# Optimization experiments

Hardware: AMD Instinct MI355X
Metric: run time of the kernel (lower is better)

Reference implementation:

```python
import jax, jax.numpy as jnp
import numpy as np

N_NODES = 20000
N_EDGES = 320000
DIMS = [256, 256, 128, 64]  # input_dim, hidden_dims...
EPS = 1e-5


def gcn_conv(x, w, b, src, dst, n):
    # PyG GCNConv: linear first, then symmetric-normalized aggregation with self-loops
    x = x @ w  # [N, out]
    loops = jnp.arange(n, dtype=src.dtype)
    src2 = jnp.concatenate([src, loops])
    dst2 = jnp.concatenate([dst, loops])
    deg = jax.ops.segment_sum(jnp.ones_like(dst2, dtype=x.dtype), dst2, num_segments=n)
    dinv = jnp.where(deg > 0, deg ** -0.5, 0.0)
    norm = dinv[src2] * dinv[dst2]  # [E+N]
    msg = x[src2] * norm[:, None]   # gathered, scaled messages
    out = jax.ops.segment_sum(msg, dst2, num_segments=n)
    return out + b


def graph_norm(x, w, b, a):
    # PyG GraphNorm over a single graph: per-feature mean/var across nodes
    mean = jnp.mean(x, axis=0)
    centered = x - a * mean
    var = jnp.mean(centered * centered, axis=0)
    return w * centered * jax.lax.rsqrt(var + EPS) + b


def layer_norm(x, w, b):
    mean = jnp.mean(x, axis=-1, keepdims=True)
    var = jnp.mean((x - mean) ** 2, axis=-1, keepdims=True)
    return (x - mean) * jax.lax.rsqrt(var + EPS) * w + b


def setup_inputs() -> dict:
    key = jax.random.key(0)
    ks = jax.random.split(key, 32)
    inp = {}
    inp["x"] = jax.random.normal(ks[0], (N_NODES, DIMS[0]), dtype=jnp.float32)
    inp["edge_index"] = jax.random.randint(ks[1], (2, N_EDGES), 0, N_NODES, dtype=jnp.int32)
    ki = 2
    for i in range(3):
        fin, fout = DIMS[i], DIMS[i + 1]
        s = 1.0 / np.sqrt(fin)
        inp[f"w{i}"] = jax.random.uniform(ks[ki], (fin, fout), jnp.float32, -s, s); ki += 1
        inp[f"b{i}"] = jnp.zeros((fout,), jnp.float32)
        inp[f"gn{i}_w"] = jnp.ones((fout,), jnp.float32)
        inp[f"gn{i}_b"] = jnp.zeros((fout,), jnp.float32)
        inp[f"gn{i}_a"] = jnp.ones((fout,), jnp.float32)
    h = DIMS[-1]
    s = 1.0 / np.sqrt(3 * h)
    inp["wc1"] = jax.random.uniform(ks[ki], (3 * h, h), jnp.float32, -s, s); ki += 1
    inp["bc1"] = jnp.zeros((h,), jnp.float32)
    inp["ln_w"] = jnp.ones((h,), jnp.float32)
    inp["ln_b"] = jnp.zeros((h,), jnp.float32)
    s = 1.0 / np.sqrt(h)
    inp["wc2"] = jax.random.uniform(ks[ki], (h, 2), jnp.float32, -s, s); ki += 1
    inp["bc2"] = jnp.zeros((2,), jnp.float32)
    return inp


def reference(x, edge_index,
              w0, b0, gn0_w, gn0_b, gn0_a,
              w1, b1, gn1_w, gn1_b, gn1_a,
              w2, b2, gn2_w, gn2_b, gn2_a,
              wc1, bc1, ln_w, ln_b, wc2, bc2):
    src, dst = edge_index[0], edge_index[1]
    n = x.shape[0]
    params = [(w0, b0, gn0_w, gn0_b, gn0_a),
              (w1, b1, gn1_w, gn1_b, gn1_a),
              (w2, b2, gn2_w, gn2_b, gn2_a)]
    for (w, b, gw, gb, ga) in params:
        x_res = x
        x = gcn_conv(x, w, b, src, dst, n)
        x = graph_norm(x, gw, gb, ga)
        x = jax.nn.gelu(x, approximate=False)
        # dropout = identity (eval); residual only when shapes match (layer 0)
        if x.shape == x_res.shape:
            x = x + x_res
    # multi-pool over the single graph (batch vector of zeros): mean | max | sum
    pooled = jnp.concatenate([jnp.mean(x, axis=0), jnp.max(x, axis=0), jnp.sum(x, axis=0)])[None, :]  # [1, 3h]
    h = pooled @ wc1 + bc1
    h = layer_norm(h, ln_w, ln_b)
    h = jax.nn.gelu(h, approximate=False)
    return h @ wc2 + bc2  # [1, num_classes]
```

## Files before the change

### kernel.cpp

```cpp
#include <hip/hip_runtime.h>
#include <math.h>

#define EPSV 1e-5f
#define MAXB 2176
#define GBLK 2080

typedef __attribute__((ext_vector_type(8))) short short8;
typedef __attribute__((ext_vector_type(4))) float f32x4;

__device__ __forceinline__ float gelu_f(float x) {
    return 0.5f * x * (1.0f + erff(x * 0.70710678118654752440f));
}

__device__ __forceinline__ float4 f4add(float4 a, float4 b) {
    return make_float4(a.x + b.x, a.y + b.y, a.z + b.z, a.w + b.w);
}

__device__ __forceinline__ ushort f2bf(float v) {
    union { float f; unsigned u; } a; a.f = v;
    unsigned r = a.u + 0x7FFFu + ((a.u >> 16) & 1u);
    return (ushort)(r >> 16);
}
__device__ __forceinline__ float bf2f(ushort h) {
    union { unsigned u; float f; } a; a.u = ((unsigned)h) << 16;
    return a.f;
}
__device__ __forceinline__ float4 bf4f(ushort4 v) {
    return make_float4(bf2f(v.x), bf2f(v.y), bf2f(v.z), bf2f(v.w));
}
__device__ __forceinline__ void f8_to_bf(const float* f, short8& h, short8& l) {
    union { short8 v; ushort u[8]; } H, L;
#pragma unroll
    for (int j = 0; j < 8; ++j) {
        H.u[j] = f2bf(f[j]);
        L.u[j] = f2bf(f[j] - bf2f(H.u[j]));
    }
    h = H.v; l = L.v;
}

__global__ void deg_kernel(const int* __restrict__ ei, int* __restrict__ deg, int E) {
    int stride = gridDim.x * blockDim.x;
    for (int e = blockIdx.x * blockDim.x + threadIdx.x; e < E; e += stride)
        atomicAdd(&deg[ei[E + e]], 1);
}

__global__ __launch_bounds__(1024) void scan_kernel(const int* __restrict__ deg,
                                                    int* __restrict__ off,
                                                    float* __restrict__ dinv, int N) {
    __shared__ int sh[1024];
    int t = threadIdx.x;
    int chunk = (N + 1023) >> 10;
    int b = t * chunk;
    int e = b + chunk; if (e > N) e = N;
    int s = 0;
    for (int i = b; i < e; ++i) s += deg[i];
    sh[t] = s;
    __syncthreads();
    for (int d = 1; d < 1024; d <<= 1) {
        int v = (t >= d) ? sh[t - d] : 0;
        __syncthreads();
        sh[t] += v;
        __syncthreads();
    }
    int run = (t > 0) ? sh[t - 1] : 0;
    for (int i = b; i < e; ++i) {
        off[i] = run;
        run += deg[i];
        dinv[i] = rsqrtf((float)(deg[i] + 1));
    }
    if (t == 1023) off[N] = sh[1023];
}

__global__ void fill_kernel(const int* __restrict__ ei, const int* __restrict__ off,
                            int* __restrict__ fill, int* __restrict__ csr, int E) {
    int stride = gridDim.x * blockDim.x;
    for (int e = blockIdx.x * blockDim.x + threadIdx.x; e < E; e += stride) {
        int d = ei[E + e];
        int p = off[d] + atomicAdd(&fill[d], 1);
        csr[p] = ei[e];
    }
}

__global__ void packw_all_kernel(const float* __restrict__ w0, const float* __restrict__ w1,
                                 const float* __restrict__ w2,
                                 ushort* __restrict__ wthi, ushort* __restrict__ wtlo)
{
    int idx = blockIdx.x * 256 + threadIdx.x;
    const float* W; int K, F, base, local;
    if (idx < 65536)       { W = w0; K = 256; F = 256; base = 0;     local = idx; }
    else if (idx < 98304)  { W = w1; K = 256; F = 128; base = 65536; local = idx - 65536; }
    else if (idx < 106496) { W = w2; K = 128; F = 64;  base = 98304; local = idx - 98304; }
    else return;
    int k = local / F, f = local - k * F;
    float v = W[local];
    ushort h = f2bf(v);
    wthi[base + f * K + k] = h;
    wtlo[base + f * K + k] = f2bf(v - bf2f(h));
}

template<int K, int BN, int MODE>
__global__ __launch_bounds__(256) void gemm_mfma_kernel(
    const float* __restrict__ axf,
    const ushort* __restrict__ tsrc,
    const float* __restrict__ tm, const float* __restrict__ tis,
    const float* __restrict__ tgw, const float* __restrict__ tgb,
    const float* __restrict__ tga, const float* __restrict__ res,
    const ushort* __restrict__ wthi, const ushort* __restrict__ wtlo,
    const float* __restrict__ dinv, ushort* __restrict__ C,
    int M, int F)
{
    constexpr int BM = 128, BK = 64;
    constexpr int LDK = BK + 8;
    constexpr int CF  = BN / 32;
    constexpr int WCH = BN / 32;

    __shared__ ushort AsH[BM * LDK], AsL[BM * LDK];
    __shared__ ushort WsH[BN * LDK], WsL[BN * LDK];

    const int tid = threadIdx.x;
    const int l = tid & 63, w = tid >> 6;
    const int wr = w >> 1, wc = w & 1;
    const int m0   = blockIdx.y * BM;
    const int colB = blockIdx.x * BN;
    const int lr = l & 15, lkg = l >> 4;

    f32x4 acc[4][CF] = {};

    for (int kk = 0; kk < K; kk += BK) {
        short8 ra[4], rb[4], rwh[WCH], rwl[WCH];
#pragma unroll
        for (int i = 0; i < 4; ++i) {
            int q = tid + i * 256;
            int row = q >> 3, cc = q & 7;
            int rg = m0 + row; if (rg > M - 1) rg = M - 1;
            int kc = kk + cc * 8;
            float y[8];
            if constexpr (MODE == 0) {
                const float* xp = axf + (size_t)rg * K + kc;
                float4 v0 = *(const float4*)xp, v1 = *(const float4*)(xp + 4);
                y[0]=v0.x; y[1]=v0.y; y[2]=v0.z; y[3]=v0.w;
                y[4]=v1.x; y[5]=v1.y; y[6]=v1.z; y[7]=v1.w;
            } else {
                const ushort* tp = tsrc + (size_t)rg * K + kc;
                float4 v0 = bf4f(*(const ushort4*)tp);
                float4 v1 = bf4f(*(const ushort4*)(tp + 4));
                float4 m0v = *(const float4*)(tm + kc),  m1v = *(const float4*)(tm + kc + 4);
                float4 i0v = *(const float4*)(tis + kc), i1v = *(const float4*)(tis + kc + 4);
                float4 w0v = *(const float4*)(tgw + kc), w1v = *(const float4*)(tgw + kc + 4);
                float4 b0v = *(const float4*)(tgb + kc), b1v = *(const float4*)(tgb + kc + 4);
                float4 a0v = *(const float4*)(tga + kc), a1v = *(const float4*)(tga + kc + 4);
                y[0] = gelu_f(w0v.x * (v0.x - a0v.x * m0v.x) * i0v.x + b0v.x);
                y[1] = gelu_f(w0v.y * (v0.y - a0v.y * m0v.y) * i0v.y + b0v.y);
                y[2] = gelu_f(w0v.z * (v0.z - a0v.z * m0v.z) * i0v.z + b0v.z);
                y[3] = gelu_f(w0v.w * (v0.w - a0v.w * m0v.w) * i0v.w + b0v.w);
                y[4] = gelu_f(w1v.x * (v1.x - a1v.x * m1v.x) * i1v.x + b1v.x);
                y[5] = gelu_f(w1v.y * (v1.y - a1v.y * m1v.y) * i1v.y + b1v.y);
                y[6] = gelu_f(w1v.z * (v1.z - a1v.z * m1v.z) * i1v.z + b1v.z);
                y[7] = gelu_f(w1v.w * (v1.w - a1v.w * m1v.w) * i1v.w + b1v.w);
                if (res) {
                    const float* rp = res + (size_t)rg * K + kc;
                    float4 r0 = *(const float4*)rp, r1 = *(const float4*)(rp + 4);
                    y[0] += r0.x; y[1] += r0.y; y[2] += r0.z; y[3] += r0.w;
                    y[4] += r1.x; y[5] += r1.y; y[6] += r1.z; y[7] += r1.w;
                }
            }
            f8_to_bf(y, ra[i], rb[i]);
        }
#pragma unroll
        for (int i = 0; i < WCH; ++i) {
            int q = tid + i * 256;
            int row = q >> 3, cc = q & 7;
            rwh[i] = *(const short8*)(wthi + (size_t)(colB + row) * K + kk + cc * 8);
            rwl[i] = *(const short8*)(wtlo + (size_t)(colB + row) * K + kk + cc * 8);
        }
        __syncthreads();
#pragma unroll
        for (int i = 0; i < 4; ++i) {
            int q = tid + i * 256;
            int row = q >> 3, cc = q & 7;
            *(short8*)&AsH[row * LDK + cc * 8] = ra[i];
            *(short8*)&AsL[row * LDK + cc * 8] = rb[i];
        }
#pragma unroll
        for (int i = 0; i < WCH; ++i) {
            int q = tid + i * 256;
            int row = q >> 3, cc = q & 7;
            *(short8*)&WsH[row * LDK + cc * 8] = rwh[i];
            *(short8*)&WsL[row * LDK + cc * 8] = rwl[i];
        }
        __syncthreads();

#pragma unroll
        for (int ks = 0; ks < 2; ++ks) {
            const int kof = ks * 32 + lkg * 8;
            short8 afh[4], afl[4];
#pragma unroll
            for (int rf = 0; rf < 4; ++rf) {
                int row = wr * 64 + rf * 16 + lr;
                afh[rf] = *(const short8*)&AsH[row * LDK + kof];
                afl[rf] = *(const short8*)&AsL[row * LDK + kof];
            }
            short8 wfh[CF], wfl[CF];
#pragma unroll
            for (int cf = 0; cf < CF; ++cf) {
                int row = wc * (BN / 2) + cf * 16 + lr;
                wfh[cf] = *(const short8*)&WsH[row * LDK + kof];
                wfl[cf] = *(const short8*)&WsL[row * LDK + kof];
            }
#pragma unroll
            for (int rf = 0; rf < 4; ++rf) {
#pragma unroll
                for (int cf = 0; cf < CF; ++cf) {
                    acc[rf][cf] = __builtin_amdgcn_mfma_f32_16x16x32_bf16(afh[rf], wfh[cf], acc[rf][cf], 0, 0, 0);
                    acc[rf][cf] = __builtin_amdgcn_mfma_f32_16x16x32_bf16(afh[rf], wfl[cf], acc[rf][cf], 0, 0, 0);
                    acc[rf][cf] = __builtin_amdgcn_mfma_f32_16x16x32_bf16(afl[rf], wfh[cf], acc[rf][cf], 0, 0, 0);
                }
            }
        }
    }

#pragma unroll
    for (int rf = 0; rf < 4; ++rf) {
#pragma unroll
        for (int j = 0; j < 4; ++j) {
            int r = m0 + wr * 64 + rf * 16 + lkg * 4 + j;
            if (r < M) {
                float dv = dinv[r];
                ushort* Cp = C + (size_t)r * F + colB + wc * (BN / 2) + lr;
#pragma unroll
                for (int cf = 0; cf < CF; ++cf)
                    Cp[cf * 16] = f2bf(acc[rf][cf][j] * dv);
            }
        }
    }
}

template<int F>
__global__ __launch_bounds__(256) void gather_kernel(
    const ushort* __restrict__ hs, const int* __restrict__ off,
    const int* __restrict__ csr, const float* __restrict__ dinv,
    const float* __restrict__ bias, ushort* __restrict__ t,
    float* __restrict__ p1, float* __restrict__ p2, int N)
{
    constexpr int NG  = F / 64;
    constexpr int NPB = 16;
    const int lane = threadIdx.x & 15;
    const int slot = threadIdx.x >> 4;

    const int xs    = blockIdx.x & 7;
    const int g     = xs % NG;
    const int r     = xs / NG;
    const int chunk = blockIdx.x >> 3;
    const int repl  = 8 / NG;
    const int nPerG = (int)(gridDim.x >> 3) * repl;
    const int j     = chunk * repl + r;

    const int col4 = g * 16 + lane;
    const int c0 = col4 * 4;
    const float4 bv = ((const float4*)bias)[col4];

    float4 a1 = make_float4(0.f, 0.f, 0.f, 0.f);
    float4 a2 = make_float4(0.f, 0.f, 0.f, 0.f);

    for (int d = j * NPB + slot; d < N; d += nPerG * NPB) {
        float4 acc = bf4f(*(const ushort4*)(hs + (size_t)d * F + c0));
        const int e0 = off[d], e1 = off[d + 1];
        int e = e0;
        for (; e + 8 <= e1; e += 8) {
            int s0 = csr[e + 0], s1 = csr[e + 1], s2 = csr[e + 2], s3 = csr[e + 3];
            int s4 = csr[e + 4], s5 = csr[e + 5], s6 = csr[e + 6], s7 = csr[e + 7];
            ushort4 v0 = *(const ushort4*)(hs + (size_t)s0 * F + c0);
            ushort4 v1 = *(const ushort4*)(hs + (size_t)s1 * F + c0);
            ushort4 v2 = *(const ushort4*)(hs + (size_t)s2 * F + c0);
            ushort4 v3 = *(const ushort4*)(hs + (size_t)s3 * F + c0);
            ushort4 v4 = *(const ushort4*)(hs + (size_t)s4 * F + c0);
            ushort4 v5 = *(const ushort4*)(hs + (size_t)s5 * F + c0);
            ushort4 v6 = *(const ushort4*)(hs + (size_t)s6 * F + c0);
            ushort4 v7 = *(const ushort4*)(hs + (size_t)s7 * F + c0);
            float4 u0 = f4add(bf4f(v0), bf4f(v1));
            float4 u1 = f4add(bf4f(v2), bf4f(v3));
            float4 u2 = f4add(bf4f(v4), bf4f(v5));
            float4 u3 = f4add(bf4f(v6), bf4f(v7));
            acc = f4add(acc, f4add(f4add(u0, u1), f4add(u2, u3)));
        }
        for (; e + 2 <= e1; e += 2) {
            int s0 = csr[e + 0], s1 = csr[e + 1];
            ushort4 v0 = *(const ushort4*)(hs + (size_t)s0 * F + c0);
            ushort4 v1 = *(const ushort4*)(hs + (size_t)s1 * F + c0);
            acc = f4add(acc, f4add(bf4f(v0), bf4f(v1)));
        }
        if (e < e1) {
            acc = f4add(acc, bf4f(*(const ushort4*)(hs + (size_t)csr[e] * F + c0)));
        }

        float dv = dinv[d];
        float4 o;
        o.x = fmaf(dv, acc.x, bv.x);
        o.y = fmaf(dv, acc.y, bv.y);
        o.z = fmaf(dv, acc.z, bv.z);
        o.w = fmaf(dv, acc.w, bv.w);
        ushort4 ov;
        ov.x = f2bf(o.x); ov.y = f2bf(o.y); ov.z = f2bf(o.z); ov.w = f2bf(o.w);
        *(ushort4*)(t + (size_t)d * F + c0) = ov;
        a1.x += o.x; a1.y += o.y; a1.z += o.z; a1.w += o.w;
        a2.x += o.x * o.x; a2.y += o.y * o.y; a2.z += o.z * o.z; a2.w += o.w * o.w;
    }

    __shared__ float red[8][256];
    red[0][threadIdx.x] = a1.x; red[1][threadIdx.x] = a1.y;
    red[2][threadIdx.x] = a1.z; red[3][threadIdx.x] = a1.w;
    red[4][threadIdx.x] = a2.x; red[5][threadIdx.x] = a2.y;
    red[6][threadIdx.x] = a2.z; red[7][threadIdx.x] = a2.w;
    __syncthreads();
    if (slot == 0) {
        float sum[8];
#pragma unroll
        for (int k = 0; k < 8; ++k) {
            float s = red[k][lane];
            for (int jj = 1; jj < NPB; ++jj) s += red[k][jj * 16 + lane];
            sum[k] = s;
        }
        ((float4*)p1)[(long)col4 * MAXB + blockIdx.x] = make_float4(sum[0], sum[1], sum[2], sum[3]);
        ((float4*)p2)[(long)col4 * MAXB + blockIdx.x] = make_float4(sum[4], sum[5], sum[6], sum[7]);
    }
}

__global__ __launch_bounds__(256) void statreduce_kernel(
    const float* __restrict__ p1, const float* __restrict__ p2,
    const float* __restrict__ ga,
    float* __restrict__ meanv, float* __restrict__ istdv,
    int nb, int N, int NG)
{
    const int c4 = blockIdx.x;
    const int g = (c4 >> 4) % NG;
    const float4* p14 = (const float4*)p1 + (long)c4 * MAXB;
    const float4* p24 = (const float4*)p2 + (long)c4 * MAXB;
    float4 a1 = make_float4(0.f, 0.f, 0.f, 0.f);
    float4 a2 = make_float4(0.f, 0.f, 0.f, 0.f);
    for (int r = threadIdx.x; r < nb; r += 256) {
        if (((r & 7) % NG) != g) continue;
        float4 v1 = p14[r];
        float4 v2 = p24[r];
        a1.x += v1.x; a1.y += v1.y; a1.z += v1.z; a1.w += v1.w;
        a2.x += v2.x; a2.y += v2.y; a2.z += v2.z; a2.w += v2.w;
    }
#pragma unroll
    for (int offv = 32; offv > 0; offv >>= 1) {
        a1.x += __shfl_down(a1.x, offv); a1.y += __shfl_down(a1.y, offv);
        a1.z += __shfl_down(a1.z, offv); a1.w += __shfl_down(a1.w, offv);
        a2.x += __shfl_down(a2.x, offv); a2.y += __shfl_down(a2.y, offv);
        a2.z += __shfl_down(a2.z, offv); a2.w += __shfl_down(a2.w, offv);
    }
    __shared__ float4 sh1[4], sh2[4];
    const int wid = threadIdx.x >> 6;
    if ((threadIdx.x & 63) == 0) { sh1[wid] = a1; sh2[wid] = a2; }
    __syncthreads();
    if (threadIdx.x == 0) {
        float4 t1 = sh1[0], t2 = sh2[0];
        for (int jj = 1; jj < 4; ++jj) {
            float4 u1 = sh1[jj], u2 = sh2[jj];
            t1.x += u1.x; t1.y += u1.y; t1.z += u1.z; t1.w += u1.w;
            t2.x += u2.x; t2.y += u2.y; t2.z += u2.z; t2.w += u2.w;
        }
        float s1a[4] = { t1.x, t1.y, t1.z, t1.w };
        float s2a[4] = { t2.x, t2.y, t2.z, t2.w };
#pragma unroll
        for (int k = 0; k < 4; ++k) {
            int c = c4 * 4 + k;
            float m = s1a[k] / (float)N;
            float a = ga[c];
            float var = s2a[k] / (float)N - 2.f * a * m * m + a * a * m * m;
            meanv[c] = m;
            istdv[c] = rsqrtf(var + EPSV);
        }
    }
}

__device__ __forceinline__ void atomicMaxFloat(float* addr, float val) {
    unsigned* ua = (unsigned*)addr;
    unsigned old = *ua;
    while (true) {
        float of = __uint_as_float(old);
        if (of >= val) break;
        unsigned assumed = old;
        old = atomicCAS(ua, assumed, __float_as_uint(val));
        if (old == assumed) break;
    }
}

__global__ void initpool_kernel(float* __restrict__ psum, float* __restrict__ pmax) {
    int t = threadIdx.x;
    psum[t] = 0.f;
    pmax[t] = -INFINITY;
}

__global__ __launch_bounds__(256) void colpool_ng_kernel(
    const ushort* __restrict__ t, const float* __restrict__ meanv,
    const float* __restrict__ istdv, const float* __restrict__ gw,
    const float* __restrict__ gb, const float* __restrict__ ga,
    float* __restrict__ psum, float* __restrict__ pmax,
    int M, int rowsPerBlock)
{
    int c = threadIdx.x & 63;
    int rl = threadIdx.x >> 6;
    int r0 = blockIdx.x * rowsPerBlock;
    int rend = r0 + rowsPerBlock; if (rend > M) rend = M;
    const float mc = meanv[c], ic = istdv[c], wc_ = gw[c], bc_ = gb[c], ac = ga[c];
    float a1 = 0.f, am = -INFINITY;
    for (int r = r0 + rl; r < rend; r += 4) {
        float v = bf2f(t[(long)r * 64 + c]);
        float y = gelu_f(wc_ * (v - ac * mc) * ic + bc_);
        a1 += y; am = fmaxf(am, y);
    }
    __shared__ float sh1[256], shm[256];
    sh1[threadIdx.x] = a1; shm[threadIdx.x] = am;
    __syncthreads();
    if (threadIdx.x < 64) {
        for (int j = 1; j < 4; ++j) {
            a1 += sh1[c + j * 64];
            am = fmaxf(am, shm[c + j * 64]);
        }
        atomicAdd(&psum[c], a1);
        atomicMaxFloat(&pmax[c], am);
    }
}

__global__ void head_kernel(const float* __restrict__ psum, const float* __restrict__ pmax,
                            const float* __restrict__ wc1, const float* __restrict__ bc1,
                            const float* __restrict__ lnw, const float* __restrict__ lnb,
                            const float* __restrict__ wc2, const float* __restrict__ bc2,
                            float* __restrict__ out, int M)
{
    __shared__ float p[192];
    int t = threadIdx.x;
    float s = psum[t];
    p[t] = s / (float)M;
    p[64 + t] = pmax[t];
    p[128 + t] = s;
    __syncthreads();
    float h = bc1[t];
    for (int k = 0; k < 192; ++k) h = fmaf(p[k], wc1[k * 64 + t], h);
    float m = h;
    for (int off = 32; off > 0; off >>= 1) m += __shfl_xor(m, off);
    m *= (1.f / 64.f);
    float d = h - m;
    float v = d * d;
    for (int off = 32; off > 0; off >>= 1) v += __shfl_xor(v, off);
    v *= (1.f / 64.f);
    float y = d * rsqrtf(v + EPSV) * lnw[t] + lnb[t];
    y = gelu_f(y);
    float o0 = y * wc2[t * 2 + 0];
    float o1 = y * wc2[t * 2 + 1];
    for (int off = 32; off > 0; off >>= 1) {
        o0 += __shfl_xor(o0, off);
        o1 += __shfl_xor(o1, off);
    }
    if (t == 0) {
        out[0] = o0 + bc2[0];
        out[1] = o1 + bc2[1];
    }
}

extern "C" void kernel_launch(void* const* d_in, const int* in_sizes, int n_in,
                              void* d_out, int out_size, void* d_ws, size_t ws_size,
                              hipStream_t stream)
{
    const float* x    = (const float*)d_in[0];
    const int*   ei   = (const int*)d_in[1];
    const float* w0   = (const float*)d_in[2];
    const float* b0   = (const float*)d_in[3];
    const float* gn0w = (const float*)d_in[4];
    const float* gn0b = (const float*)d_in[5];
    const float* gn0a = (const float*)d_in[6];
    const float* w1   = (const float*)d_in[7];
    const float* b1   = (const float*)d_in[8];
    const float* gn1w = (const float*)d_in[9];
    const float* gn1b = (const float*)d_in[10];
    const float* gn1a = (const float*)d_in[11];
    const float* w2   = (const float*)d_in[12];
    const float* b2   = (const float*)d_in[13];
    const float* gn2w = (const float*)d_in[14];
    const float* gn2b = (const float*)d_in[15];
    const float* gn2a = (const float*)d_in[16];
    const float* wc1  = (const float*)d_in[17];
    const float* bc1  = (const float*)d_in[18];
    const float* lnw  = (const float*)d_in[19];
    const float* lnb  = (const float*)d_in[20];
    const float* wc2  = (const float*)d_in[21];
    const float* bc2  = (const float*)d_in[22];

    const int N = in_sizes[0] / 256;
    const int E = in_sizes[1] / 2;

    float* ws = (float*)d_ws;
    const size_t BIG = (size_t)N * 256;
    ushort* HS   = (ushort*)ws;
    ushort* T    = (ushort*)(ws + BIG);
    float* dinv  = ws + 2 * BIG;
    int*   deg   = (int*)(dinv + N);
    int*   fill  = deg + N;
    int*   off   = fill + N;
    int*   csr   = off + N + 1;
    float* p1    = (float*)(csr + E);
    float* p2    = p1 + (size_t)64 * MAXB * 4;
    float* meanv = p2 + (size_t)64 * MAXB * 4;
    float* istdv = meanv + 256;
    float* psum  = istdv + 256;
    float* pmax  = psum + 64;
    ushort* wthi = (ushort*)(pmax + 64);
    ushort* wtlo = wthi + 106496;
    const int woff[3] = { 0, 65536, 98304 };

    hipMemsetAsync(deg, 0, (size_t)2 * N * sizeof(int), stream);
    deg_kernel<<<1024, 256, 0, stream>>>(ei, deg, E);
    scan_kernel<<<1, 1024, 0, stream>>>(deg, off, dinv, N);
    fill_kernel<<<1024, 256, 0, stream>>>(ei, off, fill, csr, E);
    packw_all_kernel<<<416, 256, 0, stream>>>(w0, w1, w2, wthi, wtlo);

    struct Layer {
        const float *b, *gw, *gb, *ga;
        int K, F;
    } L[3] = {
        { b0, gn0w, gn0b, gn0a, 256, 256 },
        { b1, gn1w, gn1b, gn1a, 256, 128 },
        { b2, gn2w, gn2b, gn2a, 128,  64 },
    };

    const int rowTiles = (N + 127) / 128;

    gemm_mfma_kernel<256, 128, 0><<<dim3(2, rowTiles), 256, 0, stream>>>(
        x, nullptr, nullptr, nullptr, nullptr, nullptr, nullptr, nullptr,
        wthi + woff[0], wtlo + woff[0], dinv, HS, N, 256);
    gather_kernel<256><<<GBLK, 256, 0, stream>>>(HS, off, csr, dinv, L[0].b, T, p1, p2, N);
    statreduce_kernel<<<64, 256, 0, stream>>>(p1, p2, L[0].ga, meanv, istdv, GBLK, N, 4);

    gemm_mfma_kernel<256, 128, 1><<<dim3(1, rowTiles), 256, 0, stream>>>(
        nullptr, T, meanv, istdv, L[0].gw, L[0].gb, L[0].ga, x,
        wthi + woff[1], wtlo + woff[1], dinv, HS, N, 128);
    gather_kernel<128><<<GBLK, 256, 0, stream>>>(HS, off, csr, dinv, L[1].b, T, p1, p2, N);
    statreduce_kernel<<<32, 256, 0, stream>>>(p1, p2, L[1].ga, meanv, istdv, GBLK, N, 2);

    gemm_mfma_kernel<128, 64, 1><<<dim3(1, rowTiles), 256, 0, stream>>>(
        nullptr, T, meanv, istdv, L[1].gw, L[1].gb, L[1].ga, nullptr,
        wthi + woff[2], wtlo + woff[2], dinv, HS, N, 64);
    gather_kernel<64><<<GBLK, 256, 0, stream>>>(HS, off, csr, dinv, L[2].b, T, p1, p2, N);
    statreduce_kernel<<<16, 256, 0, stream>>>(p1, p2, L[2].ga, meanv, istdv, GBLK, N, 1);

    initpool_kernel<<<1, 64, 0, stream>>>(psum, pmax);
    colpool_ng_kernel<<<(N + 127) / 128, 256, 0, stream>>>(
        T, meanv, istdv, L[2].gw, L[2].gb, L[2].ga, psum, pmax, N, 128);
    head_kernel<<<1, 64, 0, stream>>>(psum, pmax, wc1, bc1, lnw, lnb, wc2, bc2,
                                      (float*)d_out, N);
}
```

Measured before the change: 275.0 us.

## Drop activation low-bf16 split in GEMM and merge small setup kernels

The GEMM no longer splits activations into high and low bf16 parts. It keeps only the high part, removing one of the three MFMA products per tile along with the AsL shared buffer and its stores. Separately, the CSR fill and weight packing kernels are merged into one launch, and pool initialisation is folded into the last statreduce launch as an extra block. These cut MFMA work, LDS traffic and launch overhead, but activations now carry only bf16 precision in the matmul, which lowers accuracy.

```diff
diff --git a/kernel.cpp b/kernel.cpp
--- a/kernel.cpp
+++ b/kernel.cpp
@@ -28,14 +28,11 @@
 __device__ __forceinline__ float4 bf4f(ushort4 v) {
     return make_float4(bf2f(v.x), bf2f(v.y), bf2f(v.z), bf2f(v.w));
 }
-__device__ __forceinline__ void f8_to_bf(const float* f, short8& h, short8& l) {
-    union { short8 v; ushort u[8]; } H, L;
-#pragma unroll
-    for (int j = 0; j < 8; ++j) {
-        H.u[j] = f2bf(f[j]);
-        L.u[j] = f2bf(f[j] - bf2f(H.u[j]));
-    }
-    h = H.v; l = L.v;
+__device__ __forceinline__ short8 f8_to_bf_hi(const float* f) {
+    union { short8 v; ushort u[8]; } H;
+#pragma unroll
+    for (int j = 0; j < 8; ++j) H.u[j] = f2bf(f[j]);
+    return H.v;
 }
 
 __global__ void deg_kernel(const int* __restrict__ ei, int* __restrict__ deg, int E) {
@@ -71,31 +68,32 @@
     if (t == 1023) off[N] = sh[1023];
 }
 
-__global__ void fill_kernel(const int* __restrict__ ei, const int* __restrict__ off,
-                            int* __restrict__ fill, int* __restrict__ csr, int E) {
-    int stride = gridDim.x * blockDim.x;
-    for (int e = blockIdx.x * blockDim.x + threadIdx.x; e < E; e += stride) {
-        int d = ei[E + e];
-        int p = off[d] + atomicAdd(&fill[d], 1);
-        csr[p] = ei[e];
-    }
-}
-
-__global__ void packw_all_kernel(const float* __restrict__ w0, const float* __restrict__ w1,
-                                 const float* __restrict__ w2,
-                                 ushort* __restrict__ wthi, ushort* __restrict__ wtlo)
-{
-    int idx = blockIdx.x * 256 + threadIdx.x;
-    const float* W; int K, F, base, local;
-    if (idx < 65536)       { W = w0; K = 256; F = 256; base = 0;     local = idx; }
-    else if (idx < 98304)  { W = w1; K = 256; F = 128; base = 65536; local = idx - 65536; }
-    else if (idx < 106496) { W = w2; K = 128; F = 64;  base = 98304; local = idx - 98304; }
-    else return;
-    int k = local / F, f = local - k * F;
-    float v = W[local];
-    ushort h = f2bf(v);
-    wthi[base + f * K + k] = h;
-    wtlo[base + f * K + k] = f2bf(v - bf2f(h));
+__global__ void fill_packw_kernel(const int* __restrict__ ei, const int* __restrict__ off,
+                                  int* __restrict__ fill, int* __restrict__ csr, int E,
+                                  const float* __restrict__ w0, const float* __restrict__ w1,
+                                  const float* __restrict__ w2,
+                                  ushort* __restrict__ wthi, ushort* __restrict__ wtlo)
+{
+    if (blockIdx.x < 1024) {
+        int stride = 1024 * blockDim.x;
+        for (int e = blockIdx.x * blockDim.x + threadIdx.x; e < E; e += stride) {
+            int d = ei[E + e];
+            int p = off[d] + atomicAdd(&fill[d], 1);
+            csr[p] = ei[e];
+        }
+    } else {
+        int idx = (blockIdx.x - 1024) * 256 + threadIdx.x;
+        const float* W; int K, F, base, local;
+        if (idx < 65536)       { W = w0; K = 256; F = 256; base = 0;     local = idx; }
+        else if (idx < 98304)  { W = w1; K = 256; F = 128; base = 65536; local = idx - 65536; }
+        else if (idx < 106496) { W = w2; K = 128; F = 64;  base = 98304; local = idx - 98304; }
+        else return;
+        int k = local / F, f = local - k * F;
+        float v = W[local];
+        ushort h = f2bf(v);
+        wthi[base + f * K + k] = h;
+        wtlo[base + f * K + k] = f2bf(v - bf2f(h));
+    }
 }
 
 template<int K, int BN, int MODE>
@@ -114,7 +112,7 @@
     constexpr int CF  = BN / 32;
     constexpr int WCH = BN / 32;
 
-    __shared__ ushort AsH[BM * LDK], AsL[BM * LDK];
+    __shared__ ushort AsH[BM * LDK];
     __shared__ ushort WsH[BN * LDK], WsL[BN * LDK];
 
     const int tid = threadIdx.x;
@@ -127,7 +125,7 @@
     f32x4 acc[4][CF] = {};
 
     for (int kk = 0; kk < K; kk += BK) {
-        short8 ra[4], rb[4], rwh[WCH], rwl[WCH];
+        short8 ra[4], rwh[WCH], rwl[WCH];
 #pragma unroll
         for (int i = 0; i < 4; ++i) {
             int q = tid + i * 256;
@@ -164,7 +162,7 @@
                     y[4] += r1.x; y[5] += r1.y; y[6] += r1.z; y[7] += r1.w;
                 }
             }
-            f8_to_bf(y, ra[i], rb[i]);
+            ra[i] = f8_to_bf_hi(y);
         }
 #pragma unroll
         for (int i = 0; i < WCH; ++i) {
@@ -179,7 +177,6 @@
             int q = tid + i * 256;
             int row = q >> 3, cc = q & 7;
             *(short8*)&AsH[row * LDK + cc * 8] = ra[i];
-            *(short8*)&AsL[row * LDK + cc * 8] = rb[i];
         }
 #pragma unroll
         for (int i = 0; i < WCH; ++i) {
@@ -193,12 +190,11 @@
 #pragma unroll
         for (int ks = 0; ks < 2; ++ks) {
             const int kof = ks * 32 + lkg * 8;
-            short8 afh[4], afl[4];
+            short8 afh[4];
 #pragma unroll
             for (int rf = 0; rf < 4; ++rf) {
                 int row = wr * 64 + rf * 16 + lr;
                 afh[rf] = *(const short8*)&AsH[row * LDK + kof];
-                afl[rf] = *(const short8*)&AsL[row * LDK + kof];
             }
             short8 wfh[CF], wfl[CF];
 #pragma unroll
@@ -213,7 +209,6 @@
                 for (int cf = 0; cf < CF; ++cf) {
                     acc[rf][cf] = __builtin_amdgcn_mfma_f32_16x16x32_bf16(afh[rf], wfh[cf], acc[rf][cf], 0, 0, 0);
                     acc[rf][cf] = __builtin_amdgcn_mfma_f32_16x16x32_bf16(afh[rf], wfl[cf], acc[rf][cf], 0, 0, 0);
-                    acc[rf][cf] = __builtin_amdgcn_mfma_f32_16x16x32_bf16(afl[rf], wfh[cf], acc[rf][cf], 0, 0, 0);
                 }
             }
         }
@@ -329,8 +324,16 @@
     const float* __restrict__ p1, const float* __restrict__ p2,
     const float* __restrict__ ga,
     float* __restrict__ meanv, float* __restrict__ istdv,
-    int nb, int N, int NG)
-{
+    int nb, int N, int NG,
+    float* __restrict__ psum, float* __restrict__ pmax)
+{
+    if (psum && blockIdx.x == gridDim.x - 1) {
+        if (threadIdx.x < 64) {
+            psum[threadIdx.x] = 0.f;
+            pmax[threadIdx.x] = -INFINITY;
+        }
+        return;
+    }
     const int c4 = blockIdx.x;
     const int g = (c4 >> 4) % NG;
     const float4* p14 = (const float4*)p1 + (long)c4 * MAXB;
@@ -386,12 +389,6 @@
         old = atomicCAS(ua, assumed, __float_as_uint(val));
         if (old == assumed) break;
     }
-}
-
-__global__ void initpool_kernel(float* __restrict__ psum, float* __restrict__ pmax) {
-    int t = threadIdx.x;
-    psum[t] = 0.f;
-    pmax[t] = -INFINITY;
 }
 
 __global__ __launch_bounds__(256) void colpool_ng_kernel(
@@ -514,8 +511,7 @@
     hipMemsetAsync(deg, 0, (size_t)2 * N * sizeof(int), stream);
     deg_kernel<<<1024, 256, 0, stream>>>(ei, deg, E);
     scan_kernel<<<1, 1024, 0, stream>>>(deg, off, dinv, N);
-    fill_kernel<<<1024, 256, 0, stream>>>(ei, off, fill, csr, E);
-    packw_all_kernel<<<416, 256, 0, stream>>>(w0, w1, w2, wthi, wtlo);
+    fill_packw_kernel<<<1440, 256, 0, stream>>>(ei, off, fill, csr, E, w0, w1, w2, wthi, wtlo);
 
     struct Layer {
         const float *b, *gw, *gb, *ga;
@@ -532,21 +528,23 @@
         x, nullptr, nullptr, nullptr, nullptr, nullptr, nullptr, nullptr,
         wthi + woff[0], wtlo + woff[0], dinv, HS, N, 256);
     gather_kernel<256><<<GBLK, 256, 0, stream>>>(HS, off, csr, dinv, L[0].b, T, p1, p2, N);
-    statreduce_kernel<<<64, 256, 0, stream>>>(p1, p2, L[0].ga, meanv, istdv, GBLK, N, 4);
+    statreduce_kernel<<<64, 256, 0, stream>>>(p1, p2, L[0].ga, meanv, istdv, GBLK, N, 4,
+                                              nullptr, nullptr);
 
     gemm_mfma_kernel<256, 128, 1><<<dim3(1, rowTiles), 256, 0, stream>>>(
         nullptr, T, meanv, istdv, L[0].gw, L[0].gb, L[0].ga, x,
         wthi + woff[1], wtlo + woff[1], dinv, HS, N, 128);
     gather_kernel<128><<<GBLK, 256, 0, stream>>>(HS, off, csr, dinv, L[1].b, T, p1, p2, N);
-    statreduce_kernel<<<32, 256, 0, stream>>>(p1, p2, L[1].ga, meanv, istdv, GBLK, N, 2);
+    statreduce_kernel<<<32, 256, 0, stream>>>(p1, p2, L[1].ga, meanv, istdv, GBLK, N, 2,
+                                              nullptr, nullptr);
 
     gemm_mfma_kernel<128, 64, 1><<<dim3(1, rowTiles), 256, 0, stream>>>(
         nullptr, T, meanv, istdv, L[1].gw, L[1].gb, L[1].ga, nullptr,
         wthi + woff[2], wtlo + woff[2], dinv, HS, N, 64);
     gather_kernel<64><<<GBLK, 256, 0, stream>>>(HS, off, csr, dinv, L[2].b, T, p1, p2, N);
-    statreduce_kernel<<<16, 256, 0, stream>>>(p1, p2, L[2].ga, meanv, istdv, GBLK, N, 1);
-
-    initpool_kernel<<<1, 64, 0, stream>>>(psum, pmax);
+    statreduce_kernel<<<17, 256, 0, stream>>>(p1, p2, L[2].ga, meanv, istdv, GBLK, N, 1,
+                                              psum, pmax);
+
     colpool_ng_kernel<<<(N + 127) / 128, 256, 0, stream>>>(
         T, meanv, istdv, L[2].gw, L[2].gb, L[2].ga, psum, pmax, N, 128);
     head_kernel<<<1, 64, 0, stream>>>(psum, pmax, wc1, bc1, lnw, lnb, wc2, bc2,
```

New measurement: 267.2 us. 1.03x faster.
